# Kernel optimization log

Measured on AMD Instinct MI355X. Metric: run time of the kernel, lower is better.

## Reference

```python
import jax, jax.numpy as jnp
import numpy as np

THETA = 40.0  # Gaussian edge temperature from __init__(theta=40)


def _unfold3(x):
    """torch F.unfold(kernel=3, pad=1, stride=1) reshaped to (n, c, 9, h, w).
    Kernel positions are enumerated row-major (ki*3 + kj), matching torch."""
    n, c, h, w = x.shape
    xp = jnp.pad(x, ((0, 0), (0, 0), (1, 1), (1, 1)))
    return jnp.stack(
        [xp[:, :, ki:ki + h, kj:kj + w] for ki in range(3) for kj in range(3)],
        axis=2,
    )


def setup_inputs() -> dict:
    key = jax.random.key(0)
    k1, k2 = jax.random.split(key)
    mask = jax.random.normal(k1, (8, 19, 256, 256), dtype=jnp.float32)
    edge = jax.random.uniform(k2, (8, 1, 256, 256), dtype=jnp.float32)
    return {"mask": mask, "edge": edge, "iter_n": 2}


def reference(mask, edge, iter_n):
    max_edge = edge.max()
    # local_edge: (n, 1, 9, h, w) = center edge + 3x3 neighborhood edge
    local_edge = edge[:, :, None, :, :] + _unfold3(edge)
    # softmax over the 9 neighborhood positions (max_edge shift is a
    # softmax-invariant stabilizer, kept for faithfulness)
    weights = jax.nn.softmax(-THETA * (local_edge - max_edge), axis=2)
    # iterative edge-guided 3x3 weighted-sum stencil on the mask
    for _ in range(iter_n):
        mask = (_unfold3(mask) * weights).sum(axis=2)
    return mask
```

## Files before the change

### kernel.cpp

```cpp
#include <hip/hip_runtime.h>


#define HH 256
#define WW 256
#define NC 19
#define THETA 40.0f

__global__ __launch_bounds__(1024)
void geg_fused_kernel(const float* __restrict__ mask,
                      const float* __restrict__ edge,
                      float* __restrict__ out) {
    const int tid = threadIdx.x;
    const int ox = blockIdx.x * 32;
    const int oy = blockIdx.y * 32;
    const int n  = blockIdx.z;

    __shared__ float e_lds[36][37];
    __shared__ float m_lds[36][37];
    __shared__ float t_lds[34][36];

    const float* eptr = edge + (size_t)n * HH * WW;
    for (int i = tid; i < 36 * 36; i += 1024) {
        int y = i / 36, x = i - y * 36;
        int gy = oy + y - 2, gx = ox + x - 2;
        float v = 0.f;
        if ((unsigned)gy < HH && (unsigned)gx < WW) v = eptr[gy * WW + gx];
        e_lds[y][x] = v;
    }
    __syncthreads();

    const int yy1 = (tid >> 5) + 1, xx1 = (tid & 31) + 1;
    const bool has2 = tid < 132;
    int yy2 = 0, xx2 = 0;
    if (has2) {
        if (tid < 34)       { yy2 = 0;          xx2 = tid;       }
        else if (tid < 68)  { yy2 = 33;         xx2 = tid - 34;  }
        else if (tid < 100) { yy2 = tid - 67;   xx2 = 0;         }
        else                { yy2 = tid - 99;   xx2 = 33;        }
    }

    float wA[9], wB[9];
    {
        float lg[9], mx = -1e30f;
        #pragma unroll
        for (int k = 0; k < 9; ++k) {
            int ki = k / 3, kj = k - ki * 3;
            lg[k] = -THETA * e_lds[yy1 + ki][xx1 + kj];
            mx = fmaxf(mx, lg[k]);
        }
        float s = 0.f;
        #pragma unroll
        for (int k = 0; k < 9; ++k) { wA[k] = __expf(lg[k] - mx); s += wA[k]; }
        float inv = 1.f / s;
        #pragma unroll
        for (int k = 0; k < 9; ++k) wA[k] *= inv;
    }
    if (has2) {
        float lg[9], mx = -1e30f;
        #pragma unroll
        for (int k = 0; k < 9; ++k) {
            int ki = k / 3, kj = k - ki * 3;
            lg[k] = -THETA * e_lds[yy2 + ki][xx2 + kj];
            mx = fmaxf(mx, lg[k]);
        }
        float s = 0.f;
        #pragma unroll
        for (int k = 0; k < 9; ++k) { wB[k] = __expf(lg[k] - mx); s += wB[k]; }
        float inv = 1.f / s;
        #pragma unroll
        for (int k = 0; k < 9; ++k) wB[k] *= inv;
    }
    const int g2y = oy + yy2 - 1, g2x = ox + xx2 - 1;
    const bool v2 = has2 && (unsigned)g2y < HH && (unsigned)g2x < WW;

    const size_t img = (size_t)HH * WW;
    const float* mbase = mask + (size_t)n * NC * img;
    float*       obase = out  + (size_t)n * NC * img;
    const int goy = oy + yy1 - 1, gox = ox + xx1 - 1;

    for (int c = 0; c < NC; ++c) {
        const float* mp = mbase + (size_t)c * img;
        __syncthreads();
        for (int i = tid; i < 36 * 36; i += 1024) {
            int y = i / 36, x = i - y * 36;
            int gy = oy + y - 2, gx = ox + x - 2;
            float v = 0.f;
            if ((unsigned)gy < HH && (unsigned)gx < WW) v = mp[gy * WW + gx];
            m_lds[y][x] = v;
        }
        __syncthreads();

        {
            float s = 0.f;
            #pragma unroll
            for (int k = 0; k < 9; ++k) {
                int ki = k / 3, kj = k - ki * 3;
                s += wA[k] * m_lds[yy1 + ki][xx1 + kj];
            }
            t_lds[yy1][xx1] = s;
        }
        if (has2) {
            float s = 0.f;
            #pragma unroll
            for (int k = 0; k < 9; ++k) {
                int ki = k / 3, kj = k - ki * 3;
                s += wB[k] * m_lds[yy2 + ki][xx2 + kj];
            }
            t_lds[yy2][xx2] = v2 ? s : 0.f;
        }
        __syncthreads();

        {
            float s = 0.f;
            #pragma unroll
            for (int k = 0; k < 9; ++k) {
                int ki = k / 3, kj = k - ki * 3;
                s += wA[k] * t_lds[yy1 - 1 + ki][xx1 - 1 + kj];
            }
            obase[(size_t)c * img + (size_t)goy * WW + gox] = s;
        }
    }
}

extern "C" void kernel_launch(void* const* d_in, const int* in_sizes, int n_in,
                              void* d_out, int out_size, void* d_ws, size_t ws_size,
                              hipStream_t stream) {
    const float* mask = (const float*)d_in[0];
    const float* edge = (const float*)d_in[1];
    float* out = (float*)d_out;

    dim3 grid(WW / 32, HH / 32, 8);
    geg_fused_kernel<<<grid, 1024, 0, stream>>>(mask, edge, out);
}
```

Measured before the change: 37.16 us.

## Rewrite stencil kernel with register-blocked 4-wide pixels and prefetched channel loads

Replaces the 1024-thread LDS-staged kernel with a 256-thread kernel in which each thread computes four adjacent pixels. The first stencil pass reads the mask straight from global memory into registers with float4 loads. The next channel's data is prefetched into registers before the barrier, and a double-buffered LDS tile holds the intermediate result. The channel loop is split across two blocks per image, which doubles the grid, and edge weights are computed from global loads with the max-shift dropped. In return, register pressure rises from the four 9-weight sets, and halo pixels are loaded with uncoalesced scalar reads.

```diff
diff --git a/kernel.cpp b/kernel.cpp
--- a/kernel.cpp
+++ b/kernel.cpp
@@ -6,119 +6,194 @@
 #define NC 19
 #define THETA 40.0f
 
-__global__ __launch_bounds__(1024)
-void geg_fused_kernel(const float* __restrict__ mask,
-                      const float* __restrict__ edge,
-                      float* __restrict__ out) {
+__global__ __launch_bounds__(256, 4)
+void geg_kernel(const float* __restrict__ mask,
+                const float* __restrict__ edge,
+                float* __restrict__ out)
+{
     const int tid = threadIdx.x;
-    const int ox = blockIdx.x * 32;
-    const int oy = blockIdx.y * 32;
-    const int n  = blockIdx.z;
-
-    __shared__ float e_lds[36][37];
-    __shared__ float m_lds[36][37];
-    __shared__ float t_lds[34][36];
-
-    const float* eptr = edge + (size_t)n * HH * WW;
-    for (int i = tid; i < 36 * 36; i += 1024) {
-        int y = i / 36, x = i - y * 36;
-        int gy = oy + y - 2, gx = ox + x - 2;
-        float v = 0.f;
-        if ((unsigned)gy < HH && (unsigned)gx < WW) v = eptr[gy * WW + gx];
-        e_lds[y][x] = v;
-    }
-    __syncthreads();
-
-    const int yy1 = (tid >> 5) + 1, xx1 = (tid & 31) + 1;
-    const bool has2 = tid < 132;
-    int yy2 = 0, xx2 = 0;
-    if (has2) {
-        if (tid < 34)       { yy2 = 0;          xx2 = tid;       }
-        else if (tid < 68)  { yy2 = 33;         xx2 = tid - 34;  }
-        else if (tid < 100) { yy2 = tid - 67;   xx2 = 0;         }
-        else                { yy2 = tid - 99;   xx2 = 33;        }
-    }
-
-    float wA[9], wB[9];
+    const int ox = blockIdx.x * 32, oy = blockIdx.y * 32;
+    const int gz  = blockIdx.z;
+    const int n   = gz >> 1;
+    const int grp = gz & 1;
+    const int c0  = grp * 10;
+    const int cN  = grp ? (NC - 10) : 10;
+
+    __shared__ float t_lds[2][34][40];
+
+    const size_t img = (size_t)HH * WW;
+    const float* mbase = mask + ((size_t)n * NC + c0) * img;
+    const float* eptr  = edge + (size_t)n * img;
+
+    const int y  = tid >> 3;
+    const int j  = tid & 7;
+    const int xq = ox + 4 * j;
+    const bool pl = xq >= 1;
+    const bool pr = xq + 4 < WW;
+    const int xa = pl ? xq - 1 : 0;
+    const int xb = pr ? xq + 4 : WW - 1;
+
+    int  rof[3]; bool rok[3];
+    #pragma unroll
+    for (int ki = 0; ki < 3; ++ki) {
+        int R = oy + y - 1 + ki;
+        rok[ki] = (unsigned)R < (unsigned)HH;
+        int Rc = R < 0 ? 0 : (R >= HH ? HH - 1 : R);
+        rof[ki] = Rc * WW;
+    }
+
+    const bool hasR = tid < 132;
+    int ru = 0, rv = 0;
+    if (tid < 34)       { ru = 0;        rv = tid;      }
+    else if (tid < 68)  { ru = 33;       rv = tid - 34; }
+    else if (tid < 100) { ru = tid - 67; rv = 0;        }
+    else if (tid < 132) { ru = tid - 99; rv = 33;       }
+    const int rpy = oy + ru - 1, rpx = ox + rv - 1;
+    const bool rpix_ok = (unsigned)rpy < (unsigned)HH && (unsigned)rpx < (unsigned)WW;
+    int rco[9]; bool rcm[9];
+    #pragma unroll
+    for (int ki = 0; ki < 3; ++ki) {
+        int R = oy + ru - 2 + ki;
+        bool rvok = (unsigned)R < (unsigned)HH;
+        int Rc = R < 0 ? 0 : (R >= HH ? HH - 1 : R);
+        #pragma unroll
+        for (int kj = 0; kj < 3; ++kj) {
+            int C = ox + rv - 2 + kj;
+            bool cvok = (unsigned)C < (unsigned)WW;
+            int Cc = C < 0 ? 0 : (C >= WW ? WW - 1 : C);
+            rco[3*ki+kj] = Rc * WW + Cc;
+            rcm[3*ki+kj] = rvok && cvok;
+        }
+    }
+
+    auto ld_int = [&](const float* mp, float* a, float4* q, float* b) {
+        #pragma unroll
+        for (int ki = 0; ki < 3; ++ki) {
+            const float* rp = mp + rof[ki];
+            a[ki] = rp[xa];
+            q[ki] = *(const float4*)(rp + xq);
+            b[ki] = rp[xb];
+        }
+    };
+    auto ld_ring = [&](const float* mp, float* r) {
+        #pragma unroll
+        for (int k = 0; k < 9; ++k) r[k] = mp[rco[k]];
+    };
+
+    float wA[4][9];
     {
-        float lg[9], mx = -1e30f;
+        float w6[3][6];
+        #pragma unroll
+        for (int ki = 0; ki < 3; ++ki) {
+            const float* rp = eptr + rof[ki];
+            float a  = rp[xa];
+            float4 q = *(const float4*)(rp + xq);
+            float b  = rp[xb];
+            const bool ok = rok[ki];
+            w6[ki][0] = (ok && pl) ? a   : 0.f;
+            w6[ki][1] = ok ? q.x : 0.f;
+            w6[ki][2] = ok ? q.y : 0.f;
+            w6[ki][3] = ok ? q.z : 0.f;
+            w6[ki][4] = ok ? q.w : 0.f;
+            w6[ki][5] = (ok && pr) ? b   : 0.f;
+        }
+        #pragma unroll
+        for (int p = 0; p < 4; ++p) {
+            float s = 0.f;
+            #pragma unroll
+            for (int ki = 0; ki < 3; ++ki)
+                #pragma unroll
+                for (int kj = 0; kj < 3; ++kj) {
+                    float v = __expf(-THETA * w6[ki][p + kj]);
+                    wA[p][3*ki+kj] = v; s += v;
+                }
+            float inv = 1.f / s;
+            #pragma unroll
+            for (int k = 0; k < 9; ++k) wA[p][k] *= inv;
+        }
+    }
+    float wB[9];
+    if (hasR) {
+        float s = 0.f;
         #pragma unroll
         for (int k = 0; k < 9; ++k) {
-            int ki = k / 3, kj = k - ki * 3;
-            lg[k] = -THETA * e_lds[yy1 + ki][xx1 + kj];
-            mx = fmaxf(mx, lg[k]);
-        }
-        float s = 0.f;
-        #pragma unroll
-        for (int k = 0; k < 9; ++k) { wA[k] = __expf(lg[k] - mx); s += wA[k]; }
+            float e = rcm[k] ? eptr[rco[k]] : 0.f;
+            wB[k] = __expf(-THETA * e);
+            s += wB[k];
+        }
         float inv = 1.f / s;
         #pragma unroll
-        for (int k = 0; k < 9; ++k) wA[k] *= inv;
-    }
-    if (has2) {
-        float lg[9], mx = -1e30f;
-        #pragma unroll
-        for (int k = 0; k < 9; ++k) {
-            int ki = k / 3, kj = k - ki * 3;
-            lg[k] = -THETA * e_lds[yy2 + ki][xx2 + kj];
-            mx = fmaxf(mx, lg[k]);
-        }
-        float s = 0.f;
-        #pragma unroll
-        for (int k = 0; k < 9; ++k) { wB[k] = __expf(lg[k] - mx); s += wB[k]; }
-        float inv = 1.f / s;
-        #pragma unroll
         for (int k = 0; k < 9; ++k) wB[k] *= inv;
     }
-    const int g2y = oy + yy2 - 1, g2x = ox + xx2 - 1;
-    const bool v2 = has2 && (unsigned)g2y < HH && (unsigned)g2x < WW;
-
-    const size_t img = (size_t)HH * WW;
-    const float* mbase = mask + (size_t)n * NC * img;
-    float*       obase = out  + (size_t)n * NC * img;
-    const int goy = oy + yy1 - 1, gox = ox + xx1 - 1;
-
-    for (int c = 0; c < NC; ++c) {
-        const float* mp = mbase + (size_t)c * img;
+
+    float  ca[3], cb[3], cr[9];
+    float4 cq[3];
+    ld_int(mbase, ca, cq, cb);
+    if (hasR) ld_ring(mbase, cr);
+
+    float* op = out + ((size_t)n * NC + c0) * img + (size_t)(oy + y) * WW + xq;
+
+    for (int cc = 0; cc < cN; ++cc) {
+        const int b = cc & 1;
+
+        float o[4] = {0.f, 0.f, 0.f, 0.f};
+        #pragma unroll
+        for (int ki = 0; ki < 3; ++ki) {
+            const bool ok = rok[ki];
+            float w[6];
+            w[0] = (ok && pl) ? ca[ki] : 0.f;
+            w[1] = ok ? cq[ki].x : 0.f;
+            w[2] = ok ? cq[ki].y : 0.f;
+            w[3] = ok ? cq[ki].z : 0.f;
+            w[4] = ok ? cq[ki].w : 0.f;
+            w[5] = (ok && pr) ? cb[ki] : 0.f;
+            #pragma unroll
+            for (int p = 0; p < 4; ++p)
+                #pragma unroll
+                for (int kj = 0; kj < 3; ++kj)
+                    o[p] += wA[p][3*ki+kj] * w[p + kj];
+        }
+        *(float4*)&t_lds[b][y + 1][4*j + 4] = make_float4(o[0], o[1], o[2], o[3]);
+
+        if (hasR) {
+            float s = 0.f;
+            #pragma unroll
+            for (int k = 0; k < 9; ++k)
+                s += wB[k] * (rcm[k] ? cr[k] : 0.f);
+            t_lds[b][ru][rv + 3] = rpix_ok ? s : 0.f;
+        }
+
+        float  na[3], nb[3], nr[9];
+        float4 nq[3];
+        if (cc + 1 < cN) {
+            const float* mp = mbase + (size_t)(cc + 1) * img;
+            ld_int(mp, na, nq, nb);
+            if (hasR) ld_ring(mp, nr);
+        }
+
         __syncthreads();
-        for (int i = tid; i < 36 * 36; i += 1024) {
-            int y = i / 36, x = i - y * 36;
-            int gy = oy + y - 2, gx = ox + x - 2;
-            float v = 0.f;
-            if ((unsigned)gy < HH && (unsigned)gx < WW) v = mp[gy * WW + gx];
-            m_lds[y][x] = v;
-        }
-        __syncthreads();
-
-        {
-            float s = 0.f;
-            #pragma unroll
-            for (int k = 0; k < 9; ++k) {
-                int ki = k / 3, kj = k - ki * 3;
-                s += wA[k] * m_lds[yy1 + ki][xx1 + kj];
-            }
-            t_lds[yy1][xx1] = s;
-        }
-        if (has2) {
-            float s = 0.f;
-            #pragma unroll
-            for (int k = 0; k < 9; ++k) {
-                int ki = k / 3, kj = k - ki * 3;
-                s += wB[k] * m_lds[yy2 + ki][xx2 + kj];
-            }
-            t_lds[yy2][xx2] = v2 ? s : 0.f;
-        }
-        __syncthreads();
-
-        {
-            float s = 0.f;
-            #pragma unroll
-            for (int k = 0; k < 9; ++k) {
-                int ki = k / 3, kj = k - ki * 3;
-                s += wA[k] * t_lds[yy1 - 1 + ki][xx1 - 1 + kj];
-            }
-            obase[(size_t)c * img + (size_t)goy * WW + gox] = s;
-        }
+
+        float o2[4] = {0.f, 0.f, 0.f, 0.f};
+        #pragma unroll
+        for (int ki = 0; ki < 3; ++ki) {
+            const float* tr = &t_lds[b][y + ki][0];
+            float4 A  = *(const float4*)(tr + 4*j);
+            float4 Bq = *(const float4*)(tr + 4*j + 4);
+            float4 C  = *(const float4*)(tr + 4*j + 8);
+            float w[6] = {A.w, Bq.x, Bq.y, Bq.z, Bq.w, C.x};
+            #pragma unroll
+            for (int p = 0; p < 4; ++p)
+                #pragma unroll
+                for (int kj = 0; kj < 3; ++kj)
+                    o2[p] += wA[p][3*ki+kj] * w[p + kj];
+        }
+        *(float4*)op = make_float4(o2[0], o2[1], o2[2], o2[3]);
+        op += img;
+
+        #pragma unroll
+        for (int ki = 0; ki < 3; ++ki) { ca[ki] = na[ki]; cq[ki] = nq[ki]; cb[ki] = nb[ki]; }
+        #pragma unroll
+        for (int k = 0; k < 9; ++k) cr[k] = nr[k];
     }
 }
 
@@ -129,6 +204,6 @@
     const float* edge = (const float*)d_in[1];
     float* out = (float*)d_out;
 
-    dim3 grid(WW / 32, HH / 32, 8);
-    geg_fused_kernel<<<grid, 1024, 0, stream>>>(mask, edge, out);
+    dim3 grid(WW / 32, HH / 32, 16);
+    geg_kernel<<<grid, 256, 0, stream>>>(mask, edge, out);
 }
```

Measured after the change: 77.99 us. 2.1x slower.
